# Kernel optimization log

Measured on AMD Instinct MI355X. Metric: run time of the kernel, lower is better.

## Reference

```python
import jax, jax.numpy as jnp
import numpy as np

B, N, M, G = 2, 8192, 8192, 256
X_MIN = Y_MIN = -35.0
CELL = abs(2.0 * X_MIN / G)  # cell size, as in construct_batched_cuda_grid


def setup_inputs() -> dict:
    key = jax.random.key(0)
    k1, k2, k3, k4, k5 = jax.random.split(key, 5)
    p_i = jax.random.uniform(k1, (B, N, 3), jnp.float32, -34.0, 34.0)
    p_j = jax.random.uniform(k2, (B, M, 3), jnp.float32, -34.0, 34.0)
    mos = jax.random.normal(k3, (B, 2, G, G), jnp.float32)
    error_p_i_flow = jax.random.uniform(k4, (B, N), jnp.float32)
    nearest_flow = jax.random.randint(k5, (B, N, 1), 0, M, jnp.int32)
    return {"p_i": p_i, "mos": mos, "p_j": p_j,
            "error_p_i_flow": error_p_i_flow, "nearest_flow": nearest_flow}


def _knn1_l1(x, y):
    # brute-force 1-NN with L1 (norm=1) distance, matching knn_points(..., K=1, norm=1)
    # build (B,N,M) dist one coordinate at a time to avoid a (B,N,M,3) intermediate
    d = (jnp.abs(x[:, :, None, 0] - y[:, None, :, 0])
         + jnp.abs(x[:, :, None, 1] - y[:, None, :, 1])
         + jnp.abs(x[:, :, None, 2] - y[:, None, :, 2]))
    return jnp.min(d, axis=-1), jnp.argmin(d, axis=-1)


def reference(p_i, mos, p_j, error_p_i_flow, nearest_flow):
    # NN_loss with reduction='none' -> error_p_i_rigid = (cham_x + cham_y)/2 (needs N==M)
    cham_x, nearest_rigid = _knn1_l1(p_i, p_j)  # (B,N), (B,N)
    cham_y, _ = _knn1_l1(p_j, p_i)              # (B,M)
    error_p_i_rigid = (cham_x + cham_y) * 0.5

    dynamic = error_p_i_flow > error_p_i_rigid             # (B,N) bool
    idx = jnp.where(dynamic, nearest_flow[..., 0], nearest_rigid)  # (B,N)
    art_labels = dynamic.astype(jnp.int32)                 # (B,N) in {0,1}

    # batched gather p_j[b, idx[b]]
    p_j_by_nn = jnp.take_along_axis(p_j, idx[..., None], axis=1)  # (B,N,3)

    # construct_batched_cuda_grid: scatter labels into (B,G,G), -1 elsewhere
    shift = jnp.array([X_MIN, Y_MIN], jnp.float32)
    cell_idx = ((p_j_by_nn[:, :, :2] - shift) / CELL).astype(jnp.int32)  # (B,N,2)
    bs = jnp.repeat(jnp.arange(B), N)
    grid = -jnp.ones((B, G, G), jnp.int32)
    grid = grid.at[bs,
                   cell_idx[..., 0].reshape(-1),
                   cell_idx[..., 1].reshape(-1)].set(art_labels.reshape(-1))

    # CrossEntropyLoss(ignore_index=-1), mean over non-ignored cells
    logp = jax.nn.log_softmax(mos, axis=1)                 # (B,C,G,G)
    valid = grid >= 0
    tgt = jnp.clip(grid, 0, None)
    lp = jnp.take_along_axis(logp, tgt[:, None], axis=1)[:, 0]  # (B,G,G)
    loss = -jnp.where(valid, lp, 0.0).sum() / jnp.maximum(valid.sum(), 1).astype(lp.dtype)
    return loss
```

## Files before the change

### kernel.cpp

```cpp
#include <hip/hip_runtime.h>
#include <float.h>

#define B_ 2
#define N_ 8192
#define G_ 256
constexpr float X_MIN_F = -35.0f;
constexpr float CELL_F  = 0.2734375f;

using u64 = unsigned long long;

#define OFF_ACCUM 524288
#define OFF_PX    524352

template<int CC>
__global__ __launch_bounds__(256) void nn_kernel(const float* __restrict__ p_i,
                                                 const float* __restrict__ p_j,
                                                 u64* __restrict__ px,
                                                 float* __restrict__ py,
                                                 int* __restrict__ grid,
                                                 unsigned* __restrict__ accum)
{
    constexpr int COLS = N_ / CC;
    constexpr int NB   = 32 * CC;
    const int dir  = blockIdx.z >> 1;
    const int b    = blockIdx.z & 1;
    const int tid  = threadIdx.x;
    const int row0 = blockIdx.x * 1024 + tid * 4;
    const int c0   = blockIdx.y * COLS;

    const float* __restrict__ P = dir ? p_j : p_i;
    const float* __restrict__ Q = dir ? p_i : p_j;

    __shared__ __align__(16) float q[COLS * 3];
    for (int t = tid; t < COLS * 3 / 4; t += 256)
        ((float4*)q)[t] = ((const float4*)(Q + ((size_t)b * N_ + c0) * 3))[t];

    {
        const int lin = blockIdx.x + 8 * (blockIdx.y + CC * blockIdx.z);
        constexpr int PER = 32768 / NB;
        if (tid < PER)
            ((uint4*)grid)[lin * PER + tid] = make_uint4(~0u, ~0u, ~0u, ~0u);
        if (lin == 0 && tid < 4) accum[tid] = 0u;
    }

    const float4* pp = (const float4*)(P + ((size_t)b * N_ + row0) * 3);
    float4 r0 = pp[0], r1 = pp[1], r2 = pp[2];
    float px_[4] = {r0.x, r0.w, r1.z, r2.y};
    float py_[4] = {r0.y, r1.x, r1.w, r2.z};
    float pz_[4] = {r0.z, r1.y, r2.x, r2.w};

    float best[4]; int bidx[4];
#pragma unroll
    for (int r = 0; r < 4; r++) { best[r] = FLT_MAX; bidx[r] = c0; }

    __syncthreads();

    if (dir == 0) {
        for (int j4 = 0; j4 < COLS; j4 += 4) {
            float4 a  = *(const float4*)&q[j4 * 3];
            float4 bb = *(const float4*)&q[j4 * 3 + 4];
            float4 cc = *(const float4*)&q[j4 * 3 + 8];
            float qx[4] = {a.x, a.w, bb.z, cc.y};
            float qy[4] = {a.y, bb.x, bb.w, cc.z};
            float qz[4] = {a.z, bb.y, cc.x, cc.w};
#pragma unroll
            for (int k = 0; k < 4; k++) {
                int jj = c0 + j4 + k;
#pragma unroll
                for (int r = 0; r < 4; r++) {
                    float d = (fabsf(px_[r] - qx[k]) + fabsf(py_[r] - qy[k]))
                              + fabsf(pz_[r] - qz[k]);
                    bool lt = d < best[r];
                    best[r] = lt ? d : best[r];
                    bidx[r] = lt ? jj : bidx[r];
                }
            }
        }
        const size_t o = (size_t)blockIdx.y * (B_ * N_) + b * N_ + row0;
#pragma unroll
        for (int r = 0; r < 4; r++)
            px[o + r] = ((u64)__float_as_uint(best[r]) << 32) | (unsigned)bidx[r];
    } else {
        for (int j4 = 0; j4 < COLS; j4 += 4) {
            float4 a  = *(const float4*)&q[j4 * 3];
            float4 bb = *(const float4*)&q[j4 * 3 + 4];
            float4 cc = *(const float4*)&q[j4 * 3 + 8];
            float qx[4] = {a.x, a.w, bb.z, cc.y};
            float qy[4] = {a.y, bb.x, bb.w, cc.z};
            float qz[4] = {a.z, bb.y, cc.x, cc.w};
#pragma unroll
            for (int k = 0; k < 4; k++)
#pragma unroll
                for (int r = 0; r < 4; r++) {
                    float d = (fabsf(px_[r] - qx[k]) + fabsf(py_[r] - qy[k]))
                              + fabsf(pz_[r] - qz[k]);
                    best[r] = fminf(best[r], d);
                }
        }
        const size_t o = (size_t)blockIdx.y * (B_ * N_) + b * N_ + row0;
#pragma unroll
        for (int r = 0; r < 4; r++) py[o + r] = best[r];
    }
}

template<int CC>
__global__ __launch_bounds__(256) void reduce_scatter_kernel(
    const u64* __restrict__ px, const float* __restrict__ py,
    const float* __restrict__ flow, const int* __restrict__ nflow,
    const float* __restrict__ Pj, int* __restrict__ grid)
{
    __shared__ u64      sbx[64];
    __shared__ unsigned sby[64];
    const int tid = threadIdx.x;
    const int p   = tid & 63;
    const int g   = tid >> 6;
    constexpr int CPG = CC / 4;

    if (tid < 64) { sbx[tid] = ~0ull; sby[tid] = ~0u; }
    __syncthreads();

    const int pt = blockIdx.x * 64 + p;
    u64   bx = ~0ull;
    float by = FLT_MAX;
#pragma unroll
    for (int k = 0; k < CPG; k++) {
        int c = g * CPG + k;
        u64 v = px[(size_t)c * (B_ * N_) + pt];
        bx = v < bx ? v : bx;
        by = fminf(by, py[(size_t)c * (B_ * N_) + pt]);
    }
    atomicMin(&sbx[p], bx);
    atomicMin(&sby[p], __float_as_uint(by));
    __syncthreads();

    if (tid < 64) {
        u64 fx = sbx[tid];
        float dx = __uint_as_float((unsigned)(fx >> 32));
        float dy = __uint_as_float(sby[tid]);
        float rigid = (dx + dy) * 0.5f;

        const int i = blockIdx.x * 64 + tid;
        const int b = i >> 13;
        const int n = i & (N_ - 1);

        bool dyn  = flow[i] > rigid;
        int label = dyn ? 1 : 0;
        int idx   = dyn ? nflow[i] : (int)(unsigned)(fx & 0xFFFFFFFFull);

        const float* qp = Pj + ((size_t)b * N_ + idx) * 3;
        float xx = qp[0], yy = qp[1];

        int cx = (int)((xx - X_MIN_F) / CELL_F);
        int cy = (int)((yy - X_MIN_F) / CELL_F);

        atomicMax(&grid[(b << 16) + cx * G_ + cy], (n << 1) | label);
    }
}

__global__ __launch_bounds__(256) void ce_kernel(const float* __restrict__ mos,
                                                 const int* __restrict__ grid,
                                                 float* __restrict__ accum,
                                                 float* __restrict__ out)
{
    int i = blockIdx.x * 256 + threadIdx.x;
    float lsum = 0.0f;
    int   lcnt = 0;

    int packed = grid[i];
    if (packed >= 0) {
        int b    = i >> 16;
        int cell = i & 0xFFFF;
        float m0 = mos[((size_t)b * 2 + 0) * 65536 + cell];
        float m1 = mos[((size_t)b * 2 + 1) * 65536 + cell];
        float mx = fmaxf(m0, m1);
        float lse = logf(expf(m0 - mx) + expf(m1 - mx));
        float sh  = ((packed & 1) ? m1 : m0) - mx;
        lsum = sh - lse;
        lcnt = 1;
    }

#pragma unroll
    for (int o = 32; o > 0; o >>= 1) {
        lsum += __shfl_down(lsum, o);
        lcnt += __shfl_down(lcnt, o);
    }
    __shared__ float wsum[4];
    __shared__ int   wcnt[4];
    int wave = threadIdx.x >> 6;
    if ((threadIdx.x & 63) == 0) { wsum[wave] = lsum; wcnt[wave] = lcnt; }
    __syncthreads();
    if (threadIdx.x == 0) {
        float s = wsum[0] + wsum[1] + wsum[2] + wsum[3];
        int   c = wcnt[0] + wcnt[1] + wcnt[2] + wcnt[3];
        atomicAdd(&accum[0], s);
        atomicAdd((int*)&accum[1], c);
        __threadfence();
        unsigned t = atomicAdd((unsigned*)&accum[2], 1u);
        if (t == gridDim.x - 1) {
            float S = atomicAdd(&accum[0], 0.0f);
            int   C = atomicAdd((int*)&accum[1], 0);
            out[0] = -S / (float)(C > 0 ? C : 1);
        }
    }
}

template<int CC>
static void run(const float* p_i, const float* mos, const float* p_j,
                const float* flow, const int* nflow, float* out,
                char* ws, hipStream_t stream)
{
    int*   grid  = (int*)ws;
    float* accum = (float*)(ws + OFF_ACCUM);
    u64*   px    = (u64*)(ws + OFF_PX);
    float* py    = (float*)(ws + OFF_PX + (size_t)CC * B_ * N_ * 8);

    dim3 g(8, CC, 4);
    nn_kernel<CC><<<g, 256, 0, stream>>>(p_i, p_j, px, py, (int*)grid,
                                         (unsigned*)accum);
    reduce_scatter_kernel<CC><<<256, 256, 0, stream>>>(px, py, flow, nflow,
                                                       p_j, grid);
    ce_kernel<<<(B_ * G_ * G_) / 256, 256, 0, stream>>>(mos, grid, accum, out);
}

extern "C" void kernel_launch(void* const* d_in, const int* in_sizes, int n_in,
                              void* d_out, int out_size, void* d_ws, size_t ws_size,
                              hipStream_t stream)
{
    const float* p_i   = (const float*)d_in[0];
    const float* mos   = (const float*)d_in[1];
    const float* p_j   = (const float*)d_in[2];
    const float* flow  = (const float*)d_in[3];
    const int*   nflow = (const int*)d_in[4];
    float* out = (float*)d_out;
    char* ws = (char*)d_ws;

    if (ws_size >= OFF_PX + (size_t)32 * B_ * N_ * 12)
        run<32>(p_i, mos, p_j, flow, nflow, out, ws, stream);
    else
        run<8>(p_i, mos, p_j, flow, nflow, out, ws, stream);
}
```

Measured before the change: 137.5 us.

## Use group-of-8 min tree in NN search, recover argmin afterwards, add 64-way column split

The forward-direction nearest-neighbour loop no longer tracks the argmin per candidate. It takes the minimum over groups of 8 columns with a fminf tree, records only the best group, and then recomputes the 8 distances of that group once to find the exact index. The reverse direction also processes 8 columns per shared-memory step. A 64-way column split is added when the workspace is large enough, which raises the block count but enlarges the partial-result buffers the reduce kernel must read.

```diff
diff --git a/kernel.cpp b/kernel.cpp
--- a/kernel.cpp
+++ b/kernel.cpp
@@ -49,53 +49,75 @@
     float py_[4] = {r0.y, r1.x, r1.w, r2.z};
     float pz_[4] = {r0.z, r1.y, r2.x, r2.w};
 
-    float best[4]; int bidx[4];
-#pragma unroll
-    for (int r = 0; r < 4; r++) { best[r] = FLT_MAX; bidx[r] = c0; }
+    float best[4];
+#pragma unroll
+    for (int r = 0; r < 4; r++) best[r] = FLT_MAX;
 
     __syncthreads();
 
     if (dir == 0) {
-        for (int j4 = 0; j4 < COLS; j4 += 4) {
-            float4 a  = *(const float4*)&q[j4 * 3];
-            float4 bb = *(const float4*)&q[j4 * 3 + 4];
-            float4 cc = *(const float4*)&q[j4 * 3 + 8];
-            float qx[4] = {a.x, a.w, bb.z, cc.y};
-            float qy[4] = {a.y, bb.x, bb.w, cc.z};
-            float qz[4] = {a.z, bb.y, cc.x, cc.w};
-#pragma unroll
-            for (int k = 0; k < 4; k++) {
-                int jj = c0 + j4 + k;
-#pragma unroll
-                for (int r = 0; r < 4; r++) {
-                    float d = (fabsf(px_[r] - qx[k]) + fabsf(py_[r] - qy[k]))
-                              + fabsf(pz_[r] - qz[k]);
-                    bool lt = d < best[r];
-                    best[r] = lt ? d : best[r];
-                    bidx[r] = lt ? jj : bidx[r];
-                }
+        int gcol[4] = {0, 0, 0, 0};
+        for (int jg = 0; jg < COLS; jg += 8) {
+            const float4* qv = (const float4*)&q[jg * 3];
+            float4 v0 = qv[0], v1 = qv[1], v2 = qv[2];
+            float4 v3 = qv[3], v4 = qv[4], v5 = qv[5];
+            float qx[8] = {v0.x, v0.w, v1.z, v2.y, v3.x, v3.w, v4.z, v5.y};
+            float qy[8] = {v0.y, v1.x, v1.w, v2.z, v3.y, v4.x, v4.w, v5.z};
+            float qz[8] = {v0.z, v1.y, v2.x, v2.w, v3.z, v4.y, v5.x, v5.w};
+#pragma unroll
+            for (int r = 0; r < 4; r++) {
+                float d[8];
+#pragma unroll
+                for (int k = 0; k < 8; k++)
+                    d[k] = (fabsf(px_[r] - qx[k]) + fabsf(py_[r] - qy[k]))
+                           + fabsf(pz_[r] - qz[k]);
+                float m01 = fminf(d[0], d[1]), m23 = fminf(d[2], d[3]);
+                float m45 = fminf(d[4], d[5]), m67 = fminf(d[6], d[7]);
+                float m = fminf(fminf(m01, m23), fminf(m45, m67));
+                bool lt = m < best[r];
+                best[r] = lt ? m : best[r];
+                gcol[r] = lt ? jg : gcol[r];
             }
+        }
+        int bidx[4];
+#pragma unroll
+        for (int r = 0; r < 4; r++) {
+            const float4* qv = (const float4*)&q[gcol[r] * 3];
+            float4 v0 = qv[0], v1 = qv[1], v2 = qv[2];
+            float4 v3 = qv[3], v4 = qv[4], v5 = qv[5];
+            float qx[8] = {v0.x, v0.w, v1.z, v2.y, v3.x, v3.w, v4.z, v5.y};
+            float qy[8] = {v0.y, v1.x, v1.w, v2.z, v3.y, v4.x, v4.w, v5.z};
+            float qz[8] = {v0.z, v1.y, v2.x, v2.w, v3.z, v4.y, v5.x, v5.w};
+            int kk = 0;
+#pragma unroll
+            for (int k = 7; k >= 0; k--) {
+                float d = (fabsf(px_[r] - qx[k]) + fabsf(py_[r] - qy[k]))
+                          + fabsf(pz_[r] - qz[k]);
+                kk = (d == best[r]) ? k : kk;
+            }
+            bidx[r] = c0 + gcol[r] + kk;
         }
         const size_t o = (size_t)blockIdx.y * (B_ * N_) + b * N_ + row0;
 #pragma unroll
         for (int r = 0; r < 4; r++)
             px[o + r] = ((u64)__float_as_uint(best[r]) << 32) | (unsigned)bidx[r];
     } else {
-        for (int j4 = 0; j4 < COLS; j4 += 4) {
-            float4 a  = *(const float4*)&q[j4 * 3];
-            float4 bb = *(const float4*)&q[j4 * 3 + 4];
-            float4 cc = *(const float4*)&q[j4 * 3 + 8];
-            float qx[4] = {a.x, a.w, bb.z, cc.y};
-            float qy[4] = {a.y, bb.x, bb.w, cc.z};
-            float qz[4] = {a.z, bb.y, cc.x, cc.w};
-#pragma unroll
-            for (int k = 0; k < 4; k++)
-#pragma unroll
-                for (int r = 0; r < 4; r++) {
+        for (int jg = 0; jg < COLS; jg += 8) {
+            const float4* qv = (const float4*)&q[jg * 3];
+            float4 v0 = qv[0], v1 = qv[1], v2 = qv[2];
+            float4 v3 = qv[3], v4 = qv[4], v5 = qv[5];
+            float qx[8] = {v0.x, v0.w, v1.z, v2.y, v3.x, v3.w, v4.z, v5.y};
+            float qy[8] = {v0.y, v1.x, v1.w, v2.z, v3.y, v4.x, v4.w, v5.z};
+            float qz[8] = {v0.z, v1.y, v2.x, v2.w, v3.z, v4.y, v5.x, v5.w};
+#pragma unroll
+            for (int r = 0; r < 4; r++) {
+#pragma unroll
+                for (int k = 0; k < 8; k++) {
                     float d = (fabsf(px_[r] - qx[k]) + fabsf(py_[r] - qy[k]))
                               + fabsf(pz_[r] - qz[k]);
                     best[r] = fminf(best[r], d);
                 }
+            }
         }
         const size_t o = (size_t)blockIdx.y * (B_ * N_) + b * N_ + row0;
 #pragma unroll
@@ -234,7 +256,9 @@
     float* out = (float*)d_out;
     char* ws = (char*)d_ws;
 
-    if (ws_size >= OFF_PX + (size_t)32 * B_ * N_ * 12)
+    if (ws_size >= OFF_PX + (size_t)64 * B_ * N_ * 12)
+        run<64>(p_i, mos, p_j, flow, nflow, out, ws, stream);
+    else if (ws_size >= OFF_PX + (size_t)32 * B_ * N_ * 12)
         run<32>(p_i, mos, p_j, flow, nflow, out, ws, stream);
     else
         run<8>(p_i, mos, p_j, flow, nflow, out, ws, stream);
```

New measurement: 128.4 us. -6.6%, faster.
